# Optimization experiments

Hardware: AMD Instinct MI355X
Metric: run time of the kernel (lower is better)

The kernel has to match this reference:

```python
import jax, jax.numpy as jnp
import numpy as np


def setup_inputs() -> dict:
    key = jax.random.key(0)
    k0, k1, k2, k3 = jax.random.split(key, 4)
    B, T, C = 4, 2048, 1024
    x = jax.random.normal(k0, (B, T, C), dtype=jnp.float32)
    s = C ** -0.5  # init-scale for weights so activations stay O(1)
    Wq = jax.random.normal(k1, (C, C), dtype=jnp.float32) * s
    Wk = jax.random.normal(k2, (C, C), dtype=jnp.float32) * s
    Wv = jax.random.normal(k3, (C, C), dtype=jnp.float32) * s
    return {"x": x, "Wq": Wq, "Wk": Wk, "Wv": Wv}


def reference(x, Wq, Wk, Wv):
    B, T, C = x.shape
    # torch nn.Linear: y = x @ W.T
    q = jnp.einsum('btc,dc->btd', x, Wq)
    k = jnp.einsum('btc,dc->btd', x, Wk)
    v = jnp.einsum('btc,dc->btd', x, Wv)
    scale = C ** -0.5
    wei = jnp.einsum('btd,bsd->bts', q, k) * scale  # [B, T, T]
    causal = jnp.tril(jnp.ones((T, T), dtype=bool))
    wei = jnp.where(causal, wei, -jnp.inf)
    wei = jax.nn.softmax(wei, axis=-1)
    out = jnp.einsum('bts,bsd->btd', wei, v)
    return out
```

## Files before the change

### kernel.cpp

```cpp
#include <hip/hip_runtime.h>
#include <hip/hip_bf16.h>
#include <math.h>

#define B_ 4
#define T_ 2048
#define C_ 1024
#define M_ (B_*T_)

typedef __attribute__((ext_vector_type(8))) __bf16 bf16x8;
typedef __attribute__((ext_vector_type(4))) float floatx4;

__device__ inline float bf2f(unsigned short u){
    return __uint_as_float(((unsigned)u) << 16);
}
__device__ inline unsigned short f2bf(float f){
    unsigned u = __float_as_uint(f);
    unsigned r = (u + 0x7fffu + ((u >> 16) & 1u)) >> 16;
    return (unsigned short)r;
}

__device__ inline void llds16(const unsigned short* g, unsigned short* lds){
    __builtin_amdgcn_global_load_lds(
        (const __attribute__((address_space(1))) unsigned int*)g,
        (__attribute__((address_space(3))) unsigned int*)(unsigned int)(uintptr_t)lds,
        16, 0, 0);
}

#define NX_ (M_*C_/4)
#define NW_ (C_*C_/4)
#define NL4_ (M_/4)
__global__ __launch_bounds__(256) void cast_all(
    const float* __restrict__ x, const float* __restrict__ wq,
    const float* __restrict__ wk, const float* __restrict__ wv,
    unsigned short* __restrict__ xb, unsigned short* __restrict__ wb,
    float* __restrict__ l)
{
    int i = blockIdx.x * 256 + threadIdx.x;
    const float* src; unsigned short* dst; int idx;
    if (i < NX_){ src = x; dst = xb; idx = i; }
    else if (i < NX_ + 3 * NW_){
        i -= NX_;
        int w = i / NW_; idx = i - w * NW_;
        src = (w == 0) ? wq : ((w == 1) ? wk : wv);
        dst = wb + (size_t)w * C_ * C_;
    } else {
        ((float4*)l)[i - NX_ - 3 * NW_] = make_float4(0.f, 0.f, 0.f, 0.f);
        return;
    }
    float4 v = ((const float4*)src)[idx];
    ((ushort4*)dst)[idx] = make_ushort4(f2bf(v.x), f2bf(v.y), f2bf(v.z), f2bf(v.w));
}

template<int WM, int WN>
__device__ inline void gemm_core(const unsigned short* __restrict__ A,
                                 const unsigned short* __restrict__ Bm,
                                 int lda, int ldb, int m0, int n0, int kTiles,
                                 unsigned short* As, unsigned short* Bs,
                                 floatx4 (*acc)[WN/16])
{
    const int tid  = threadIdx.x;
    const int lane = tid & 63;
    const int wave = tid >> 6;
    const int wm = (wave >> 1) * WM;
    const int wn = (wave & 1) * WN;
    const int fr = lane & 15;
    const int fq = lane >> 4;
    const int cxor = fr & 7;
    const int sr = lane >> 3;
    const int sc = ((lane & 7) ^ ((lane >> 3) & 7)) * 8;

    const unsigned short* gA = A  + (size_t)(m0 + wave * (WM/2) + sr) * lda + sc;
    const unsigned short* gB = Bm + (size_t)(n0 + wave * (WN/2) + sr) * ldb + sc;
    unsigned short* ldsA = As + wave * (WM/2) * 64;
    unsigned short* ldsB = Bs + wave * (WN/2) * 64;

    for (int kt = 0; kt < kTiles; kt++){
        const int k0 = kt * 64;
        __syncthreads();
        #pragma unroll
        for (int i = 0; i < WM/16; i++)
            llds16(gA + (size_t)(i * 8) * lda + k0, ldsA + i * 8 * 64);
        #pragma unroll
        for (int i = 0; i < WN/16; i++)
            llds16(gB + (size_t)(i * 8) * ldb + k0, ldsB + i * 8 * 64);
        __syncthreads();
        #pragma unroll
        for (int ks = 0; ks < 64; ks += 32){
            const int cpos = (((ks >> 3) + fq) ^ cxor) * 8;
            bf16x8 af[WM/16], bv[WN/16];
            #pragma unroll
            for (int i = 0; i < WM/16; i++)
                af[i] = *(const bf16x8*)(As + (wm + i*16 + fr) * 64 + cpos);
            #pragma unroll
            for (int j = 0; j < WN/16; j++)
                bv[j] = *(const bf16x8*)(Bs + (wn + j*16 + fr) * 64 + cpos);
            #pragma unroll
            for (int i = 0; i < WM/16; i++)
                #pragma unroll
                for (int j = 0; j < WN/16; j++)
                    acc[i][j] = __builtin_amdgcn_mfma_f32_16x16x32_bf16(af[i], bv[j], acc[i][j], 0, 0, 0);
        }
    }
}

__global__ __launch_bounds__(256, 4) void proj_gemm(
    const unsigned short* __restrict__ xb,
    const unsigned short* __restrict__ Wb,
    unsigned short* __restrict__ Qb, unsigned short* __restrict__ Kb,
    unsigned short* __restrict__ Vt)
{
    __shared__ unsigned short As[128 * 64];
    __shared__ unsigned short Bs[128 * 64];
    const int L = blockIdx.x;
    const int k = L & 7, j = L >> 3;
    const int m0 = (k * 8 + (j & 7)) * 128;
    const int n0 = ((j >> 3) & 7) * 128;
    const int z  = j >> 6;
    const unsigned short* W = Wb + (size_t)z * C_ * C_;

    floatx4 acc[4][4];
    #pragma unroll
    for (int i = 0; i < 4; i++)
        #pragma unroll
        for (int jj = 0; jj < 4; jj++) acc[i][jj] = (floatx4){0.f,0.f,0.f,0.f};
    gemm_core<64, 64>(xb, W, C_, C_, m0, n0, C_ / 64, As, Bs, acc);

    const int lane = threadIdx.x & 63, wave = threadIdx.x >> 6;
    const int wm = (wave >> 1) * 64, wn = (wave & 1) * 64;
    const int fr = lane & 15, fq = lane >> 4;

    if (z < 2){
        unsigned short* Y = z ? Kb : Qb;
        #pragma unroll
        for (int i = 0; i < 4; i++)
            #pragma unroll
            for (int jj = 0; jj < 4; jj++)
                #pragma unroll
                for (int r = 0; r < 4; r++){
                    int row = m0 + wm + i*16 + fq*4 + r;
                    int col = n0 + wn + jj*16 + fr;
                    Y[(size_t)row * C_ + col] = f2bf(acc[i][jj][r]);
                }
    } else {
        #pragma unroll
        for (int i = 0; i < 4; i++)
            #pragma unroll
            for (int jj = 0; jj < 4; jj++){
                int row = m0 + wm + i*16 + fq*4;
                int col = n0 + wn + jj*16 + fr;
                int b = row / T_, t = row % T_;
                ushort4 o = make_ushort4(f2bf(acc[i][jj][0]), f2bf(acc[i][jj][1]),
                                         f2bf(acc[i][jj][2]), f2bf(acc[i][jj][3]));
                *(ushort4*)&Vt[(size_t)b * C_ * T_ + (size_t)col * T_ + t] = o;
            }
    }
}

__global__ __launch_bounds__(256, 4) void score_gemm(
    const unsigned short* __restrict__ Qb, const unsigned short* __restrict__ Kb,
    unsigned short* __restrict__ P, float* __restrict__ l)
{
    const int L = blockIdx.x;
    const int xcd = L & 7, j = L >> 3;
    const int b  = xcd >> 1;
    const int p  = j / 34, rem = j % 34;
    const int th = rem & 1, rr = rem >> 1;
    const int kk = 2 * p + (xcd & 1);
    int ti, si;
    if (rr <= 15 - kk){ ti = 15 - kk; si = rr; }
    else              { ti = kk;      si = rr - (16 - kk); }
    const int t0 = ti * 128 + th * 64, s0 = si * 128;

    __shared__ unsigned short As[64 * 64];
    __shared__ unsigned short Bs[128 * 64];
    floatx4 acc[2][4];
    #pragma unroll
    for (int i = 0; i < 2; i++)
        #pragma unroll
        for (int jj = 0; jj < 4; jj++) acc[i][jj] = (floatx4){0.f,0.f,0.f,0.f};
    gemm_core<32, 64>(Qb + (size_t)b * T_ * C_, Kb + (size_t)b * T_ * C_,
                      C_, C_, t0, s0, C_ / 64, As, Bs, acc);

    const int lane = threadIdx.x & 63, wave = threadIdx.x >> 6;
    const int wm = (wave >> 1) * 32, wn = (wave & 1) * 64;
    const int fr = lane & 15, fq = lane >> 4;
    unsigned short* Pb = P + (size_t)b * T_ * T_;
    const float scale = 0.03125f;
    float rsl[2][4];
    #pragma unroll
    for (int i = 0; i < 2; i++)
        #pragma unroll
        for (int r2 = 0; r2 < 4; r2++) rsl[i][r2] = 0.f;

    #pragma unroll
    for (int i = 0; i < 2; i++)
        #pragma unroll
        for (int jj = 0; jj < 4; jj++)
            #pragma unroll
            for (int r2 = 0; r2 < 4; r2++){
                int t = t0 + wm + i*16 + fq*4 + r2;
                int s = s0 + wn + jj*16 + fr;
                float v = (s <= t) ? __expf(acc[i][jj][r2] * scale) : 0.f;
                rsl[i][r2] += v;
                Pb[(size_t)t * T_ + s] = f2bf(v);
            }
    #pragma unroll
    for (int i = 0; i < 2; i++)
        #pragma unroll
        for (int r2 = 0; r2 < 4; r2++){
            float v = rsl[i][r2];
            v += __shfl_xor(v, 1, 64);
            v += __shfl_xor(v, 2, 64);
            v += __shfl_xor(v, 4, 64);
            v += __shfl_xor(v, 8, 64);
            if (fr == 0){
                int t = t0 + wm + i*16 + fq*4 + r2;
                atomicAdd(&l[(size_t)b * T_ + t], v);
            }
        }
}

__global__ __launch_bounds__(256, 4) void pv_gemm(
    const unsigned short* __restrict__ P, const unsigned short* __restrict__ Vt,
    const float* __restrict__ l, float* __restrict__ out)
{
    const int L = blockIdx.x;
    const int xcd = L & 7, j = L >> 3;
    const int b  = xcd >> 1;
    const int p  = j >> 4;
    const int n0 = (j & 15) * 64;
    const int kk = 2 * p + (xcd & 1);

    __shared__ unsigned short As[128 * 64];
    __shared__ unsigned short Bs[64 * 64];

    const int lane = threadIdx.x & 63, wave = threadIdx.x >> 6;
    const int wm = (wave >> 1) * 64, wn = (wave & 1) * 32;
    const int fr = lane & 15, fq = lane >> 4;
    float* ob = out + (size_t)b * T_ * C_;
    const float* lb = l + (size_t)b * T_;

    #pragma unroll
    for (int phase = 0; phase < 2; phase++){
        const int ti = phase ? kk : (15 - kk);
        const int t0 = ti * 128;
        const int kTiles = 2 * (ti + 1);

        floatx4 acc[4][2];
        #pragma unroll
        for (int i = 0; i < 4; i++)
            #pragma unroll
            for (int jj = 0; jj < 2; jj++) acc[i][jj] = (floatx4){0.f,0.f,0.f,0.f};
        gemm_core<64, 32>(P + (size_t)b * T_ * T_, Vt + (size_t)b * C_ * T_,
                          T_, T_, t0, n0, kTiles, As, Bs, acc);

        #pragma unroll
        for (int i = 0; i < 4; i++){
            float inv[4];
            #pragma unroll
            for (int r2 = 0; r2 < 4; r2++)
                inv[r2] = 1.f / lb[t0 + wm + i*16 + fq*4 + r2];
            #pragma unroll
            for (int jj = 0; jj < 2; jj++)
                #pragma unroll
                for (int r2 = 0; r2 < 4; r2++){
                    int t = t0 + wm + i*16 + fq*4 + r2;
                    int d = n0 + wn + jj*16 + fr;
                    ob[(size_t)t * C_ + d] = acc[i][jj][r2] * inv[r2];
                }
        }
    }
}

extern "C" void kernel_launch(void* const* d_in, const int* in_sizes, int n_in,
                              void* d_out, int out_size, void* d_ws, size_t ws_size,
                              hipStream_t stream)
{
    const float* x  = (const float*)d_in[0];
    const float* Wq = (const float*)d_in[1];
    const float* Wk = (const float*)d_in[2];
    const float* Wv = (const float*)d_in[3];
    float* out = (float*)d_out;

    unsigned short* Qb = (unsigned short*)d_ws;
    unsigned short* Kb = Qb + (size_t)M_ * C_;
    unsigned short* Vt = Kb + (size_t)M_ * C_;
    unsigned short* P  = Vt + (size_t)M_ * C_;
    float* l = (float*)(P + (size_t)M_ * T_);
    unsigned short* xb = P;
    unsigned short* Wb = P + (size_t)M_ * C_;

    cast_all<<<(NX_ + 3 * NW_ + NL4_ + 255) / 256, 256, 0, stream>>>(
        x, Wq, Wk, Wv, xb, Wb, l);
    proj_gemm <<<1536, 256, 0, stream>>>(xb, Wb, Qb, Kb, Vt);
    score_gemm<<<1088, 256, 0, stream>>>(Qb, Kb, P, l);
    pv_gemm   <<<512,  256, 0, stream>>>(P, Vt, l, out);
}
```

Baseline: 201.0 us.

## Use 8-wave 512-thread blocks with larger tiles for projection and score GEMMs

Adds an 8-wave GEMM core and moves the projection GEMM to 256x128 tiles and the score GEMM to 128x128 tiles, using 512-thread blocks and half as many blocks. The larger tiles let each block reuse shared-memory B (and A) tiles across more waves, cutting global-to-LDS traffic per output. The cost is more LDS and registers per block, which may lower occupancy, and fewer blocks for load balancing.

```diff
diff --git a/kernel.cpp b/kernel.cpp
--- a/kernel.cpp
+++ b/kernel.cpp
@@ -103,19 +103,71 @@
     }
 }
 
-__global__ __launch_bounds__(256, 4) void proj_gemm(
+template<int WM, int WN>
+__device__ inline void gemm_core8(const unsigned short* __restrict__ A,
+                                  const unsigned short* __restrict__ Bm,
+                                  int lda, int ldb, int m0, int n0, int kTiles,
+                                  unsigned short* As, unsigned short* Bs,
+                                  floatx4 (*acc)[WN/16])
+{
+    const int tid  = threadIdx.x;
+    const int lane = tid & 63;
+    const int wave = tid >> 6;
+    const int wm = (wave >> 1) * WM;
+    const int wn = (wave & 1) * WN;
+    const int fr = lane & 15;
+    const int fq = lane >> 4;
+    const int cxor = fr & 7;
+    const int sr = lane >> 3;
+    const int sc = ((lane & 7) ^ ((lane >> 3) & 7)) * 8;
+
+    const unsigned short* gA = A  + (size_t)(m0 + wave * (WM/2) + sr) * lda + sc;
+    const unsigned short* gB = Bm + (size_t)(n0 + wave * (WN/4) + sr) * ldb + sc;
+    unsigned short* ldsA = As + wave * (WM/2) * 64;
+    unsigned short* ldsB = Bs + wave * (WN/4) * 64;
+
+    for (int kt = 0; kt < kTiles; kt++){
+        const int k0 = kt * 64;
+        __syncthreads();
+        #pragma unroll
+        for (int i = 0; i < WM/16; i++)
+            llds16(gA + (size_t)(i * 8) * lda + k0, ldsA + i * 8 * 64);
+        #pragma unroll
+        for (int i = 0; i < WN/32; i++)
+            llds16(gB + (size_t)(i * 8) * ldb + k0, ldsB + i * 8 * 64);
+        __syncthreads();
+        #pragma unroll
+        for (int ks = 0; ks < 64; ks += 32){
+            const int cpos = (((ks >> 3) + fq) ^ cxor) * 8;
+            bf16x8 af[WM/16], bv[WN/16];
+            #pragma unroll
+            for (int i = 0; i < WM/16; i++)
+                af[i] = *(const bf16x8*)(As + (wm + i*16 + fr) * 64 + cpos);
+            #pragma unroll
+            for (int j = 0; j < WN/16; j++)
+                bv[j] = *(const bf16x8*)(Bs + (wn + j*16 + fr) * 64 + cpos);
+            #pragma unroll
+            for (int i = 0; i < WM/16; i++)
+                #pragma unroll
+                for (int j = 0; j < WN/16; j++)
+                    acc[i][j] = __builtin_amdgcn_mfma_f32_16x16x32_bf16(af[i], bv[j], acc[i][j], 0, 0, 0);
+        }
+    }
+}
+
+__global__ __launch_bounds__(512, 6) void proj_gemm(
     const unsigned short* __restrict__ xb,
     const unsigned short* __restrict__ Wb,
     unsigned short* __restrict__ Qb, unsigned short* __restrict__ Kb,
     unsigned short* __restrict__ Vt)
 {
-    __shared__ unsigned short As[128 * 64];
+    __shared__ unsigned short As[256 * 64];
     __shared__ unsigned short Bs[128 * 64];
     const int L = blockIdx.x;
     const int k = L & 7, j = L >> 3;
-    const int m0 = (k * 8 + (j & 7)) * 128;
-    const int n0 = ((j >> 3) & 7) * 128;
-    const int z  = j >> 6;
+    const int m0 = (k * 4 + (j & 3)) * 256;
+    const int n0 = ((j >> 2) & 7) * 128;
+    const int z  = j >> 5;
     const unsigned short* W = Wb + (size_t)z * C_ * C_;
 
     floatx4 acc[4][4];
@@ -123,7 +175,7 @@
     for (int i = 0; i < 4; i++)
         #pragma unroll
         for (int jj = 0; jj < 4; jj++) acc[i][jj] = (floatx4){0.f,0.f,0.f,0.f};
-    gemm_core<64, 64>(xb, W, C_, C_, m0, n0, C_ / 64, As, Bs, acc);
+    gemm_core8<64, 64>(xb, W, C_, C_, m0, n0, C_ / 64, As, Bs, acc);
 
     const int lane = threadIdx.x & 63, wave = threadIdx.x >> 6;
     const int wm = (wave >> 1) * 64, wn = (wave & 1) * 64;
@@ -156,30 +208,29 @@
     }
 }
 
-__global__ __launch_bounds__(256, 4) void score_gemm(
+__global__ __launch_bounds__(512, 4) void score_gemm(
     const unsigned short* __restrict__ Qb, const unsigned short* __restrict__ Kb,
     unsigned short* __restrict__ P, float* __restrict__ l)
 {
     const int L = blockIdx.x;
     const int xcd = L & 7, j = L >> 3;
     const int b  = xcd >> 1;
-    const int p  = j / 34, rem = j % 34;
-    const int th = rem & 1, rr = rem >> 1;
+    const int p  = j / 17, rr = j % 17;
     const int kk = 2 * p + (xcd & 1);
     int ti, si;
     if (rr <= 15 - kk){ ti = 15 - kk; si = rr; }
     else              { ti = kk;      si = rr - (16 - kk); }
-    const int t0 = ti * 128 + th * 64, s0 = si * 128;
-
-    __shared__ unsigned short As[64 * 64];
+    const int t0 = ti * 128, s0 = si * 128;
+
+    __shared__ unsigned short As[128 * 64];
     __shared__ unsigned short Bs[128 * 64];
     floatx4 acc[2][4];
     #pragma unroll
     for (int i = 0; i < 2; i++)
         #pragma unroll
         for (int jj = 0; jj < 4; jj++) acc[i][jj] = (floatx4){0.f,0.f,0.f,0.f};
-    gemm_core<32, 64>(Qb + (size_t)b * T_ * C_, Kb + (size_t)b * T_ * C_,
-                      C_, C_, t0, s0, C_ / 64, As, Bs, acc);
+    gemm_core8<32, 64>(Qb + (size_t)b * T_ * C_, Kb + (size_t)b * T_ * C_,
+                       C_, C_, t0, s0, C_ / 64, As, Bs, acc);
 
     const int lane = threadIdx.x & 63, wave = threadIdx.x >> 6;
     const int wm = (wave >> 1) * 32, wn = (wave & 1) * 64;
@@ -292,7 +343,7 @@
 
     cast_all<<<(NX_ + 3 * NW_ + NL4_ + 255) / 256, 256, 0, stream>>>(
         x, Wq, Wk, Wv, xb, Wb, l);
-    proj_gemm <<<1536, 256, 0, stream>>>(xb, Wb, Qb, Kb, Vt);
-    score_gemm<<<1088, 256, 0, stream>>>(Qb, Kb, P, l);
-    pv_gemm   <<<512,  256, 0, stream>>>(P, Vt, l, out);
-}
+    proj_gemm <<<768, 512, 0, stream>>>(xb, Wb, Qb, Kb, Vt);
+    score_gemm<<<544, 512, 0, stream>>>(Qb, Kb, P, l);
+    pv_gemm   <<<512, 256, 0, stream>>>(P, Vt, l, out);
+}
```

Result: slower. 516.6 us (+157.0%).
